# Kernel tuning notes

Hardware: AMD Instinct MI355X
Metric: run time of the kernel (lower is better)

Reference implementation:

```python
import jax, jax.numpy as jnp
import numpy as np

N_NODES = 100000
N_EDGES = 1600000
IN_CH, HID_CH, OUT_CH = 128, 128, 64


def setup_inputs() -> dict:
    key = jax.random.key(0)
    ks = jax.random.split(key, 9)
    x = jax.random.normal(ks[0], (N_NODES, IN_CH), dtype=jnp.float32)
    edge_index = jax.random.randint(ks[1], (2, N_EDGES), 0, N_NODES, dtype=jnp.int64)
    def glorot(k, shape):
        fan_in = shape[1]
        return jax.random.normal(k, shape, dtype=jnp.float32) / jnp.sqrt(jnp.float32(fan_in))
    return {
        "x": x,
        "edge_index": edge_index,
        "W1_l": glorot(ks[2], (HID_CH, IN_CH)),
        "W1_r": glorot(ks[3], (HID_CH, IN_CH)),
        "b1": jnp.zeros((HID_CH,), jnp.float32),
        "W2_l": glorot(ks[4], (HID_CH, HID_CH)),
        "W2_r": glorot(ks[5], (HID_CH, HID_CH)),
        "b2": jnp.zeros((HID_CH,), jnp.float32),
        "W3_l": glorot(ks[6], (OUT_CH, HID_CH)),
        "W3_r": glorot(ks[7], (OUT_CH, HID_CH)),
        "b3": jnp.zeros((OUT_CH,), jnp.float32),
    }


def _sage_conv(x, src, dst, W_l, W_r, b):
    # PyG SAGEConv (aggr='mean', root_weight=True): out = lin_l(mean_j x_j) + lin_r(x_i)
    n = x.shape[0]
    msg = x[src]                                            # [E, C] gather at source
    agg = jax.ops.segment_sum(msg, dst, num_segments=n)     # [N, C] scatter-sum at dest
    cnt = jax.ops.segment_sum(jnp.ones((src.shape[0],), x.dtype), dst, num_segments=n)
    mean = agg / jnp.maximum(cnt, 1.0)[:, None]             # zero-in-degree nodes -> 0
    return mean @ W_l.T + x @ W_r.T + b


def reference(x, edge_index, W1_l, W1_r, b1, W2_l, W2_r, b2, W3_l, W3_r, b3):
    src, dst = edge_index[0], edge_index[1]
    h = jax.nn.relu(_sage_conv(x, src, dst, W1_l, W1_r, b1))
    # F.dropout with training=False is identity (eval mode)
    h = jax.nn.relu(_sage_conv(h, src, dst, W2_l, W2_r, b2))
    return _sage_conv(h, src, dst, W3_l, W3_r, b3)
```

## Files before the change

kernel.cpp:

```cpp
#include <hip/hip_runtime.h>
#include <hip/hip_bf16.h>
#include <cstddef>
#include <cstdint>

#define NBLK(n, b) (((n) + (b) - 1) / (b))

typedef __attribute__((ext_vector_type(8))) short short8;
typedef __attribute__((ext_vector_type(4))) float f32x4;

__device__ inline unsigned short f2bf(float f) {
  union { float f; unsigned u; } v; v.f = f;
  unsigned u = v.u;
  u += 0x7FFFu + ((u >> 16) & 1u);
  return (unsigned short)(u >> 16);
}
__device__ inline float bflo(unsigned u) { union { unsigned u; float f; } v; v.u = u << 16; return v.f; }
__device__ inline float bfhi(unsigned u) { union { unsigned u; float f; } v; v.u = u & 0xFFFF0000u; return v.f; }

#define BSHIFT 9
#define BSIZE 512


__device__ inline void prep_w_dev(const float* __restrict__ Wl, const float* __restrict__ Wr,
                                  unsigned short* __restrict__ Wb, int b) {
  int i = b * 256 + threadIdx.x;
  int nrow = i >> 8, k = i & 255;
  float v = (k < 128) ? Wr[nrow * 128 + k] : Wl[nrow * 128 + (k - 128)];
  Wb[i] = f2bf(v);
}

__global__ void k_setup(const float* __restrict__ x, unsigned* __restrict__ xb, int N,
                        int* __restrict__ bucketCnt, int NB,
                        const float* __restrict__ W1l, const float* __restrict__ W1r, unsigned short* __restrict__ Wb1,
                        const float* __restrict__ W2l, const float* __restrict__ W2r, unsigned short* __restrict__ Wb2,
                        const float* __restrict__ W3l, const float* __restrict__ W3r, unsigned short* __restrict__ Wb3,
                        const unsigned* __restrict__ edges, int* __restrict__ flag) {
  int b = blockIdx.x;
  int gCast = (N * 64 + 255) >> 8;
  if (b < gCast) {
    int i = b * 256 + threadIdx.x;
    if (i < N * 64) {
      float2 v = *(const float2*)(x + (size_t)i * 2);
      xb[i] = (unsigned)f2bf(v.x) | ((unsigned)f2bf(v.y) << 16);
    }
    return;
  }
  b -= gCast;
  if (b < 128) { prep_w_dev(W1l, W1r, Wb1, b); return; }
  b -= 128;
  if (b < 128) { prep_w_dev(W2l, W2r, Wb2, b); return; }
  b -= 128;
  if (b < 64) { prep_w_dev(W3l, W3r, Wb3, b); return; }
  b -= 64;
  if (b == 0) {
    for (int i = threadIdx.x; i < NB; i += 256) bucketCnt[i] = 0;
    if (threadIdx.x == 0) {
      int is64 = 1;
#pragma unroll
      for (int i = 0; i < 16; ++i)
        if (edges[2 * i + 1] != 0u) is64 = 0;
      *flag = is64;
    }
  }
}


__global__ __launch_bounds__(256) void k_bhist(const void* __restrict__ edges, const int* __restrict__ flag,
                                               int* __restrict__ bucketCnt, int E, int NB) {
  __shared__ int h[1024];
  for (int i = threadIdx.x; i < NB; i += 256) h[i] = 0;
  __syncthreads();
  int base_e = blockIdx.x * 4096;
  bool is64 = (*flag) != 0;
#pragma unroll
  for (int k = 0; k < 16; ++k) {
    int e = base_e + k * 256 + threadIdx.x;
    if (e < E) {
      int d;
      if (is64) d = (int)((const long long*)edges)[(size_t)E + e];
      else      d = ((const int*)edges)[(size_t)E + e];
      atomicAdd(&h[d >> BSHIFT], 1);
    }
  }
  __syncthreads();
  for (int i = threadIdx.x; i < NB; i += 256) {
    int c = h[i];
    if (c) atomicAdd(&bucketCnt[i], c);
  }
}

__global__ void k_bscan(const int* __restrict__ bucketCnt, int* __restrict__ bucketBase,
                        int* __restrict__ bucketCursor, int NB, int E) {
  __shared__ int sd[256];
  int t = threadIdx.x;
  int base = t * 4;
  int v[4];
  int sum = 0;
#pragma unroll
  for (int i = 0; i < 4; ++i) {
    int idx = base + i;
    v[i] = (idx < NB) ? bucketCnt[idx] : 0;
    sum += v[i];
  }
  sd[t] = sum;
  __syncthreads();
  for (int off = 1; off < 256; off <<= 1) {
    int xv = (t >= off) ? sd[t - off] : 0;
    __syncthreads();
    sd[t] += xv;
    __syncthreads();
  }
  int run = sd[t] - sum;
#pragma unroll
  for (int i = 0; i < 4; ++i) {
    int idx = base + i;
    if (idx < NB) { bucketBase[idx] = run; bucketCursor[idx] = run; }
    run += v[i];
  }
  if (t == 0) bucketBase[NB] = E;
}

__global__ __launch_bounds__(256) void k_bscatter(const void* __restrict__ edges, const int* __restrict__ flag,
                                                  int* __restrict__ bucketCursor, unsigned* __restrict__ bucketed,
                                                  int E, int NB) {
  __shared__ int h[1024];
  __shared__ int base[1024];
  for (int i = threadIdx.x; i < NB; i += 256) h[i] = 0;
  __syncthreads();
  int base_e = blockIdx.x * 4096;
  bool is64 = (*flag) != 0;
  unsigned key[16];
  int bkt[16];
#pragma unroll
  for (int k = 0; k < 16; ++k) {
    int e = base_e + k * 256 + threadIdx.x;
    bkt[k] = -1;
    if (e < E) {
      int s, d;
      if (is64) {
        s = (int)((const long long*)edges)[e];
        d = (int)((const long long*)edges)[(size_t)E + e];
      } else {
        s = ((const int*)edges)[e];
        d = ((const int*)edges)[(size_t)E + e];
      }
      bkt[k] = d >> BSHIFT;
      key[k] = (unsigned)s | ((unsigned)(d & (BSIZE - 1)) << 17);
      atomicAdd(&h[bkt[k]], 1);
    }
  }
  __syncthreads();
  for (int i = threadIdx.x; i < NB; i += 256) {
    int c = h[i];
    base[i] = c ? atomicAdd(&bucketCursor[i], c) : 0;
    h[i] = 0;
  }
  __syncthreads();
#pragma unroll
  for (int k = 0; k < 16; ++k) {
    if (bkt[k] >= 0) {
      int r = atomicAdd(&h[bkt[k]], 1);
      bucketed[base[bkt[k]] + r] = key[k];
    }
  }
}

__global__ __launch_bounds__(256) void k_csr(const unsigned* __restrict__ bucketed,
                                             const int* __restrict__ bucketBase,
                                             int* __restrict__ rowptr, int* __restrict__ srcSorted,
                                             int N, int E, int NB) {
  __shared__ int h[512];
  __shared__ int excl[512];
  __shared__ int sd[256];
  int b = blockIdx.x;
  int t = threadIdx.x;
  int nodeBase = b << BSHIFT;
  int nNode = min(BSIZE, N - nodeBase);
  int s0 = bucketBase[b], s1 = bucketBase[b + 1];
  int cnt = s1 - s0;
  h[t * 2] = 0; h[t * 2 + 1] = 0;
  __syncthreads();
  for (int i = t; i < cnt; i += 256) {
    int ld = bucketed[s0 + i] >> 17;
    atomicAdd(&h[ld], 1);
  }
  __syncthreads();
  int a0 = h[t * 2], a1 = h[t * 2 + 1];
  int s = a0 + a1;
  sd[t] = s;
  __syncthreads();
  for (int off = 1; off < 256; off <<= 1) {
    int xv = (t >= off) ? sd[t - off] : 0;
    __syncthreads();
    sd[t] += xv;
    __syncthreads();
  }
  int run = sd[t] - s;
  excl[t * 2] = run;
  excl[t * 2 + 1] = run + a0;
  if (t * 2 < nNode) rowptr[nodeBase + t * 2] = s0 + run;
  if (t * 2 + 1 < nNode) rowptr[nodeBase + t * 2 + 1] = s0 + run + a0;
  if (b == NB - 1 && t == 0) rowptr[N] = E;
  h[t * 2] = 0; h[t * 2 + 1] = 0;
  __syncthreads();
  for (int i = t; i < cnt; i += 256) {
    unsigned u = bucketed[s0 + i];
    int ld = u >> 17;
    int r = atomicAdd(&h[ld], 1);
    srcSorted[s0 + excl[ld] + r] = (int)(u & 0x1FFFFu);
  }
}

__global__ void k_aggregate(const unsigned* __restrict__ in, const int* __restrict__ rowptr,
                            const int* __restrict__ srcs, unsigned* __restrict__ mean, int n) {
  int lane = threadIdx.x & 63;
  int w = threadIdx.x >> 6;
  int node = blockIdx.x * 4 + w;
  if (node >= n) return;
  int r0 = rowptr[node], r1 = rowptr[node + 1];
  int sub = lane & 15;
  int eg = lane >> 4;
  float acc[8];
#pragma unroll
  for (int k = 0; k < 8; ++k) acc[k] = 0.f;

  for (int base = r0; base < r1; base += 64) {
    int e = base + lane;
    int sv = (e < r1) ? srcs[e] : 0;
    int cnt = min(64, r1 - base);
    int j = 0;
    for (; j + 8 <= cnt; j += 8) {
      int s0 = __shfl(sv, j + eg);
      int s1 = __shfl(sv, j + 4 + eg);
      uint4 u0 = *(const uint4*)(in + (size_t)s0 * 64 + sub * 4);
      uint4 u1 = *(const uint4*)(in + (size_t)s1 * 64 + sub * 4);
      acc[0] += bflo(u0.x); acc[1] += bfhi(u0.x);
      acc[2] += bflo(u0.y); acc[3] += bfhi(u0.y);
      acc[4] += bflo(u0.z); acc[5] += bfhi(u0.z);
      acc[6] += bflo(u0.w); acc[7] += bfhi(u0.w);
      acc[0] += bflo(u1.x); acc[1] += bfhi(u1.x);
      acc[2] += bflo(u1.y); acc[3] += bfhi(u1.y);
      acc[4] += bflo(u1.z); acc[5] += bfhi(u1.z);
      acc[6] += bflo(u1.w); acc[7] += bfhi(u1.w);
    }
    for (; j < cnt; j += 4) {
      int jj = j + eg;
      int s = __shfl(sv, jj);
      if (jj < cnt) {
        uint4 u = *(const uint4*)(in + (size_t)s * 64 + sub * 4);
        acc[0] += bflo(u.x); acc[1] += bfhi(u.x);
        acc[2] += bflo(u.y); acc[3] += bfhi(u.y);
        acc[4] += bflo(u.z); acc[5] += bfhi(u.z);
        acc[6] += bflo(u.w); acc[7] += bfhi(u.w);
      }
    }
  }

#pragma unroll
  for (int k = 0; k < 8; ++k) {
    acc[k] += __shfl_down(acc[k], 32);
    acc[k] += __shfl_down(acc[k], 16);
  }
  if (eg == 0) {
    float sc = 1.0f / (float)max(r1 - r0, 1);
    uint4 o;
    o.x = (unsigned)f2bf(acc[0] * sc) | ((unsigned)f2bf(acc[1] * sc) << 16);
    o.y = (unsigned)f2bf(acc[2] * sc) | ((unsigned)f2bf(acc[3] * sc) << 16);
    o.z = (unsigned)f2bf(acc[4] * sc) | ((unsigned)f2bf(acc[5] * sc) << 16);
    o.w = (unsigned)f2bf(acc[6] * sc) | ((unsigned)f2bf(acc[7] * sc) << 16);
    *(uint4*)(mean + (size_t)node * 64 + sub * 4) = o;
  }
}

template <int H, bool RELU, bool BF16OUT>
__global__ __launch_bounds__(256) void k_gemm(
    const unsigned short* __restrict__ selfB, const unsigned short* __restrict__ meanB,
    const unsigned short* __restrict__ Wb, const float* __restrict__ bias,
    void* __restrict__ outp, int n) {
  constexpr int TN = H / 32;
  int lane = threadIdx.x & 63;
  int w = threadIdx.x >> 6;
  int wr = w & 1, wc = w >> 1;
  int nodeBase = blockIdx.x * 128 + wr * 64;
  int colBase = wc * (H / 2);
  int l15 = lane & 15, quad = lane >> 4;

  f32x4 acc[4][TN];
#pragma unroll
  for (int t = 0; t < 4; ++t)
#pragma unroll
    for (int j = 0; j < TN; ++j) acc[t][j] = (f32x4){0.f, 0.f, 0.f, 0.f};

#pragma unroll
  for (int c = 0; c < 8; ++c) {
    const unsigned short* A = (c < 4) ? selfB : meanB;
    int ko = (c & 3) * 32 + quad * 8;
    short8 af[4], bfr[TN];
#pragma unroll
    for (int t = 0; t < 4; ++t) {
      int row = nodeBase + t * 16 + l15;
      row = min(row, n - 1);
      af[t] = *(const short8*)(A + (size_t)row * 128 + ko);
    }
#pragma unroll
    for (int j = 0; j < TN; ++j) {
      int cn = colBase + j * 16 + l15;
      bfr[j] = *(const short8*)(Wb + (size_t)cn * 256 + c * 32 + quad * 8);
    }
#pragma unroll
    for (int t = 0; t < 4; ++t)
#pragma unroll
      for (int j = 0; j < TN; ++j)
        acc[t][j] = __builtin_amdgcn_mfma_f32_16x16x32_bf16(af[t], bfr[j], acc[t][j], 0, 0, 0);
  }

#pragma unroll
  for (int j = 0; j < TN; ++j) {
    int col = colBase + j * 16 + l15;
    float bv = bias[col];
#pragma unroll
    for (int t = 0; t < 4; ++t) {
#pragma unroll
      for (int r = 0; r < 4; ++r) {
        int row = nodeBase + t * 16 + quad * 4 + r;
        if (row < n) {
          float v = acc[t][j][r] + bv;
          if (RELU) v = fmaxf(v, 0.f);
          if (BF16OUT) ((unsigned short*)outp)[(size_t)row * H + col] = f2bf(v);
          else ((float*)outp)[(size_t)row * H + col] = v;
        }
      }
    }
  }
}


extern "C" void kernel_launch(void* const* d_in, const int* in_sizes, int n_in,
                              void* d_out, int out_size, void* d_ws, size_t ws_size,
                              hipStream_t stream) {
  (void)n_in; (void)out_size; (void)ws_size;
  const float* x = (const float*)d_in[0];
  const void* edges = d_in[1];
  const float* W1l = (const float*)d_in[2];
  const float* W1r = (const float*)d_in[3];
  const float* b1 = (const float*)d_in[4];
  const float* W2l = (const float*)d_in[5];
  const float* W2r = (const float*)d_in[6];
  const float* b2 = (const float*)d_in[7];
  const float* W3l = (const float*)d_in[8];
  const float* W3r = (const float*)d_in[9];
  const float* b3 = (const float*)d_in[10];
  float* out = (float*)d_out;

  const int N = in_sizes[0] / 128;
  const int E = in_sizes[1] / 2;
  const int NB = (N + BSIZE - 1) >> BSHIFT;

  char* ws = (char*)d_ws;
  size_t off = 0;
  auto alloc = [&](size_t bytes) -> char* {
    char* p = ws + off;
    off = (off + bytes + 255) & ~(size_t)255;
    return p;
  };
  int* flag = (int*)alloc(4);
  int* bucketCnt = (int*)alloc((size_t)NB * 4);
  int* bucketBase = (int*)alloc((size_t)(NB + 1) * 4);
  int* bucketCursor = (int*)alloc((size_t)NB * 4);
  unsigned* bucketed = (unsigned*)alloc((size_t)E * 4);
  int* rowptr = (int*)alloc((size_t)(N + 1) * 4);
  int* srcSorted = (int*)alloc((size_t)E * 4);
  unsigned short* xb = (unsigned short*)alloc((size_t)N * 128 * 2);
  unsigned short* mean = (unsigned short*)alloc((size_t)N * 128 * 2);
  unsigned short* h1 = (unsigned short*)alloc((size_t)N * 128 * 2);
  unsigned short* h2 = (unsigned short*)alloc((size_t)N * 128 * 2);
  unsigned short* Wb1 = (unsigned short*)alloc(128 * 256 * 2);
  unsigned short* Wb2 = (unsigned short*)alloc(128 * 256 * 2);
  unsigned short* Wb3 = (unsigned short*)alloc(64 * 256 * 2);

  int gSetup = NBLK(N * 64, 256) + 128 + 128 + 64 + 1;
  int gE = NBLK(E, 4096);

  k_setup<<<gSetup, 256, 0, stream>>>(x, (unsigned*)xb, N, bucketCnt, NB,
                                      W1l, W1r, Wb1, W2l, W2r, Wb2, W3l, W3r, Wb3,
                                      (const unsigned*)edges, flag);
  k_bhist<<<gE, 256, 0, stream>>>(edges, flag, bucketCnt, E, NB);
  k_bscan<<<1, 256, 0, stream>>>(bucketCnt, bucketBase, bucketCursor, NB, E);
  k_bscatter<<<gE, 256, 0, stream>>>(edges, flag, bucketCursor, bucketed, E, NB);
  k_csr<<<NB, 256, 0, stream>>>(bucketed, bucketBase, rowptr, srcSorted, N, E, NB);

  int gAgg = NBLK(N, 4);
  int gGemm = NBLK(N, 128);

  k_aggregate<<<gAgg, 256, 0, stream>>>((const unsigned*)xb, rowptr, srcSorted, (unsigned*)mean, N);
  k_gemm<128, true, true><<<gGemm, 256, 0, stream>>>(xb, mean, Wb1, b1, h1, N);
  k_aggregate<<<gAgg, 256, 0, stream>>>((const unsigned*)h1, rowptr, srcSorted, (unsigned*)mean, N);
  k_gemm<128, true, true><<<gGemm, 256, 0, stream>>>(h1, mean, Wb2, b2, h2, N);
  k_aggregate<<<gAgg, 256, 0, stream>>>((const unsigned*)h2, rowptr, srcSorted, (unsigned*)mean, N);
  k_gemm<64, false, false><<<gGemm, 256, 0, stream>>>(h2, mean, Wb3, b3, out, N);
}
```

Baseline: 472.5 us.

## Fuse CSR build stages into one cooperative kernel with grid syncs

Merges setup, bucket histogram, scan, scatter and CSR construction into a single cooperative kernel separated by grid-wide barriers. Each block keeps its per-bucket histogram and keys in registers and shared memory between phases, so the edges are read once instead of twice. This removes several kernel launches and one pass over the edge list, at the cost of a grid size fixed to the edge chunk count, which must stay co-resident. The aggregation loop also gains a 16-wide unrolled gather to keep more loads in flight.

```diff
diff --git a/kernel.cpp b/kernel.cpp
--- a/kernel.cpp
+++ b/kernel.cpp
@@ -1,7 +1,10 @@
 #include <hip/hip_runtime.h>
 #include <hip/hip_bf16.h>
+#include <hip/hip_cooperative_groups.h>
 #include <cstddef>
 #include <cstdint>
+
+namespace cg = cooperative_groups;
 
 #define NBLK(n, b) (((n) + (b) - 1) / (b))
 
@@ -19,121 +22,60 @@
 
 #define BSHIFT 9
 #define BSIZE 512
-
-
-__device__ inline void prep_w_dev(const float* __restrict__ Wl, const float* __restrict__ Wr,
-                                  unsigned short* __restrict__ Wb, int b) {
-  int i = b * 256 + threadIdx.x;
-  int nrow = i >> 8, k = i & 255;
-  float v = (k < 128) ? Wr[nrow * 128 + k] : Wl[nrow * 128 + (k - 128)];
-  Wb[i] = f2bf(v);
-}
-
-__global__ void k_setup(const float* __restrict__ x, unsigned* __restrict__ xb, int N,
-                        int* __restrict__ bucketCnt, int NB,
-                        const float* __restrict__ W1l, const float* __restrict__ W1r, unsigned short* __restrict__ Wb1,
-                        const float* __restrict__ W2l, const float* __restrict__ W2r, unsigned short* __restrict__ Wb2,
-                        const float* __restrict__ W3l, const float* __restrict__ W3r, unsigned short* __restrict__ Wb3,
-                        const unsigned* __restrict__ edges, int* __restrict__ flag) {
-  int b = blockIdx.x;
-  int gCast = (N * 64 + 255) >> 8;
-  if (b < gCast) {
-    int i = b * 256 + threadIdx.x;
-    if (i < N * 64) {
-      float2 v = *(const float2*)(x + (size_t)i * 2);
-      xb[i] = (unsigned)f2bf(v.x) | ((unsigned)f2bf(v.y) << 16);
-    }
-    return;
-  }
-  b -= gCast;
-  if (b < 128) { prep_w_dev(W1l, W1r, Wb1, b); return; }
-  b -= 128;
-  if (b < 128) { prep_w_dev(W2l, W2r, Wb2, b); return; }
-  b -= 128;
-  if (b < 64) { prep_w_dev(W3l, W3r, Wb3, b); return; }
-  b -= 64;
-  if (b == 0) {
-    for (int i = threadIdx.x; i < NB; i += 256) bucketCnt[i] = 0;
-    if (threadIdx.x == 0) {
-      int is64 = 1;
-#pragma unroll
-      for (int i = 0; i < 16; ++i)
-        if (edges[2 * i + 1] != 0u) is64 = 0;
-      *flag = is64;
-    }
-  }
-}
-
-
-__global__ __launch_bounds__(256) void k_bhist(const void* __restrict__ edges, const int* __restrict__ flag,
-                                               int* __restrict__ bucketCnt, int E, int NB) {
+#define ECHUNK 4096
+
+__global__ __launch_bounds__(256, 2) void k_build(
+    const float* __restrict__ x, unsigned* __restrict__ xb, int N,
+    const float* __restrict__ W1l, const float* __restrict__ W1r, unsigned short* __restrict__ Wb1,
+    const float* __restrict__ W2l, const float* __restrict__ W2r, unsigned short* __restrict__ Wb2,
+    const float* __restrict__ W3l, const float* __restrict__ W3r, unsigned short* __restrict__ Wb3,
+    const void* __restrict__ edges, int* __restrict__ flag,
+    int* __restrict__ bucketCnt, int* __restrict__ bucketBase, int* __restrict__ bucketCursor,
+    unsigned* __restrict__ bucketed, int* __restrict__ rowptr, int* __restrict__ srcSorted,
+    int E, int NB) {
+  cg::grid_group grid = cg::this_grid();
   __shared__ int h[1024];
-  for (int i = threadIdx.x; i < NB; i += 256) h[i] = 0;
-  __syncthreads();
-  int base_e = blockIdx.x * 4096;
-  bool is64 = (*flag) != 0;
-#pragma unroll
-  for (int k = 0; k < 16; ++k) {
-    int e = base_e + k * 256 + threadIdx.x;
-    if (e < E) {
-      int d;
-      if (is64) d = (int)((const long long*)edges)[(size_t)E + e];
-      else      d = ((const int*)edges)[(size_t)E + e];
-      atomicAdd(&h[d >> BSHIFT], 1);
-    }
-  }
-  __syncthreads();
-  for (int i = threadIdx.x; i < NB; i += 256) {
-    int c = h[i];
-    if (c) atomicAdd(&bucketCnt[i], c);
-  }
-}
-
-__global__ void k_bscan(const int* __restrict__ bucketCnt, int* __restrict__ bucketBase,
-                        int* __restrict__ bucketCursor, int NB, int E) {
+  __shared__ int base2[1024];
   __shared__ int sd[256];
   int t = threadIdx.x;
-  int base = t * 4;
-  int v[4];
-  int sum = 0;
-#pragma unroll
-  for (int i = 0; i < 4; ++i) {
-    int idx = base + i;
-    v[i] = (idx < NB) ? bucketCnt[idx] : 0;
-    sum += v[i];
-  }
-  sd[t] = sum;
+  int gid = blockIdx.x * 256 + t;
+  int gstride = gridDim.x * 256;
+
+  for (int i = gid; i < N * 64; i += gstride) {
+    float2 v = *(const float2*)(x + (size_t)i * 2);
+    xb[i] = (unsigned)f2bf(v.x) | ((unsigned)f2bf(v.y) << 16);
+  }
+  for (int i = gid; i < 320 * 256; i += gstride) {
+    const float *Wl, *Wr; unsigned short* Wb; int ii = i;
+    if (ii < 128 * 256) { Wl = W1l; Wr = W1r; Wb = Wb1; }
+    else if (ii < 256 * 256) { Wl = W2l; Wr = W2r; Wb = Wb2; ii -= 128 * 256; }
+    else { Wl = W3l; Wr = W3r; Wb = Wb3; ii -= 256 * 256; }
+    int nrow = ii >> 8, k = ii & 255;
+    float v = (k < 128) ? Wr[nrow * 128 + k] : Wl[nrow * 128 + (k - 128)];
+    Wb[ii] = f2bf(v);
+  }
+  if (blockIdx.x == 0) {
+    for (int i = t; i < NB; i += 256) bucketCnt[i] = 0;
+    if (t == 0) {
+      const unsigned* e32 = (const unsigned*)edges;
+      int is64 = 1;
+#pragma unroll
+      for (int i = 0; i < 16; ++i)
+        if (e32[2 * i + 1] != 0u) is64 = 0;
+      *flag = is64;
+    }
+  }
+  grid.sync();
+
+  bool is64 = (*flag) != 0;
+  for (int i = t; i < NB; i += 256) h[i] = 0;
   __syncthreads();
-  for (int off = 1; off < 256; off <<= 1) {
-    int xv = (t >= off) ? sd[t - off] : 0;
-    __syncthreads();
-    sd[t] += xv;
-    __syncthreads();
-  }
-  int run = sd[t] - sum;
-#pragma unroll
-  for (int i = 0; i < 4; ++i) {
-    int idx = base + i;
-    if (idx < NB) { bucketBase[idx] = run; bucketCursor[idx] = run; }
-    run += v[i];
-  }
-  if (t == 0) bucketBase[NB] = E;
-}
-
-__global__ __launch_bounds__(256) void k_bscatter(const void* __restrict__ edges, const int* __restrict__ flag,
-                                                  int* __restrict__ bucketCursor, unsigned* __restrict__ bucketed,
-                                                  int E, int NB) {
-  __shared__ int h[1024];
-  __shared__ int base[1024];
-  for (int i = threadIdx.x; i < NB; i += 256) h[i] = 0;
-  __syncthreads();
-  int base_e = blockIdx.x * 4096;
-  bool is64 = (*flag) != 0;
+  int base_e = blockIdx.x * ECHUNK;
   unsigned key[16];
   int bkt[16];
 #pragma unroll
   for (int k = 0; k < 16; ++k) {
-    int e = base_e + k * 256 + threadIdx.x;
+    int e = base_e + k * 256 + t;
     bkt[k] = -1;
     if (e < E) {
       int s, d;
@@ -150,9 +92,44 @@
     }
   }
   __syncthreads();
-  for (int i = threadIdx.x; i < NB; i += 256) {
+  for (int i = t; i < NB; i += 256) {
     int c = h[i];
-    base[i] = c ? atomicAdd(&bucketCursor[i], c) : 0;
+    if (c) atomicAdd(&bucketCnt[i], c);
+  }
+  grid.sync();
+
+  if (blockIdx.x == 0) {
+    int base = t * 4;
+    int v[4];
+    int sum = 0;
+#pragma unroll
+    for (int i = 0; i < 4; ++i) {
+      int idx = base + i;
+      v[i] = (idx < NB) ? bucketCnt[idx] : 0;
+      sum += v[i];
+    }
+    sd[t] = sum;
+    __syncthreads();
+    for (int off = 1; off < 256; off <<= 1) {
+      int xv = (t >= off) ? sd[t - off] : 0;
+      __syncthreads();
+      sd[t] += xv;
+      __syncthreads();
+    }
+    int run = sd[t] - sum;
+#pragma unroll
+    for (int i = 0; i < 4; ++i) {
+      int idx = base + i;
+      if (idx < NB) { bucketBase[idx] = run; bucketCursor[idx] = run; }
+      run += v[i];
+    }
+    if (t == 0) bucketBase[NB] = E;
+  }
+  grid.sync();
+
+  for (int i = t; i < NB; i += 256) {
+    int c = h[i];
+    base2[i] = c ? atomicAdd(&bucketCursor[i], c) : 0;
     h[i] = 0;
   }
   __syncthreads();
@@ -160,54 +137,48 @@
   for (int k = 0; k < 16; ++k) {
     if (bkt[k] >= 0) {
       int r = atomicAdd(&h[bkt[k]], 1);
-      bucketed[base[bkt[k]] + r] = key[k];
-    }
-  }
-}
-
-__global__ __launch_bounds__(256) void k_csr(const unsigned* __restrict__ bucketed,
-                                             const int* __restrict__ bucketBase,
-                                             int* __restrict__ rowptr, int* __restrict__ srcSorted,
-                                             int N, int E, int NB) {
-  __shared__ int h[512];
-  __shared__ int excl[512];
-  __shared__ int sd[256];
+      bucketed[base2[bkt[k]] + r] = key[k];
+    }
+  }
+  grid.sync();
+
   int b = blockIdx.x;
-  int t = threadIdx.x;
-  int nodeBase = b << BSHIFT;
-  int nNode = min(BSIZE, N - nodeBase);
-  int s0 = bucketBase[b], s1 = bucketBase[b + 1];
-  int cnt = s1 - s0;
-  h[t * 2] = 0; h[t * 2 + 1] = 0;
-  __syncthreads();
-  for (int i = t; i < cnt; i += 256) {
-    int ld = bucketed[s0 + i] >> 17;
-    atomicAdd(&h[ld], 1);
-  }
-  __syncthreads();
-  int a0 = h[t * 2], a1 = h[t * 2 + 1];
-  int s = a0 + a1;
-  sd[t] = s;
-  __syncthreads();
-  for (int off = 1; off < 256; off <<= 1) {
-    int xv = (t >= off) ? sd[t - off] : 0;
+  if (b < NB) {
+    int nodeBase = b << BSHIFT;
+    int nNode = min(BSIZE, N - nodeBase);
+    int s0 = bucketBase[b], s1 = bucketBase[b + 1];
+    int cnt = s1 - s0;
+    h[t * 2] = 0; h[t * 2 + 1] = 0;
     __syncthreads();
-    sd[t] += xv;
+    for (int i = t; i < cnt; i += 256) {
+      int ld = bucketed[s0 + i] >> 17;
+      atomicAdd(&h[ld], 1);
+    }
     __syncthreads();
-  }
-  int run = sd[t] - s;
-  excl[t * 2] = run;
-  excl[t * 2 + 1] = run + a0;
-  if (t * 2 < nNode) rowptr[nodeBase + t * 2] = s0 + run;
-  if (t * 2 + 1 < nNode) rowptr[nodeBase + t * 2 + 1] = s0 + run + a0;
-  if (b == NB - 1 && t == 0) rowptr[N] = E;
-  h[t * 2] = 0; h[t * 2 + 1] = 0;
-  __syncthreads();
-  for (int i = t; i < cnt; i += 256) {
-    unsigned u = bucketed[s0 + i];
-    int ld = u >> 17;
-    int r = atomicAdd(&h[ld], 1);
-    srcSorted[s0 + excl[ld] + r] = (int)(u & 0x1FFFFu);
+    int a0 = h[t * 2], a1 = h[t * 2 + 1];
+    int s = a0 + a1;
+    sd[t] = s;
+    __syncthreads();
+    for (int off = 1; off < 256; off <<= 1) {
+      int xv = (t >= off) ? sd[t - off] : 0;
+      __syncthreads();
+      sd[t] += xv;
+      __syncthreads();
+    }
+    int run = sd[t] - s;
+    base2[t * 2] = run;
+    base2[t * 2 + 1] = run + a0;
+    if (t * 2 < nNode) rowptr[nodeBase + t * 2] = s0 + run;
+    if (t * 2 + 1 < nNode) rowptr[nodeBase + t * 2 + 1] = s0 + run + a0;
+    if (b == NB - 1 && t == 0) rowptr[N] = E;
+    h[t * 2] = 0; h[t * 2 + 1] = 0;
+    __syncthreads();
+    for (int i = t; i < cnt; i += 256) {
+      unsigned u = bucketed[s0 + i];
+      int ld = u >> 17;
+      int r = atomicAdd(&h[ld], 1);
+      srcSorted[s0 + base2[ld] + r] = (int)(u & 0x1FFFFu);
+    }
   }
 }
 
@@ -229,6 +200,32 @@
     int sv = (e < r1) ? srcs[e] : 0;
     int cnt = min(64, r1 - base);
     int j = 0;
+    for (; j + 16 <= cnt; j += 16) {
+      int s0 = __shfl(sv, j + eg);
+      int s1 = __shfl(sv, j + 4 + eg);
+      int s2 = __shfl(sv, j + 8 + eg);
+      int s3 = __shfl(sv, j + 12 + eg);
+      uint4 u0 = *(const uint4*)(in + (size_t)s0 * 64 + sub * 4);
+      uint4 u1 = *(const uint4*)(in + (size_t)s1 * 64 + sub * 4);
+      uint4 u2 = *(const uint4*)(in + (size_t)s2 * 64 + sub * 4);
+      uint4 u3 = *(const uint4*)(in + (size_t)s3 * 64 + sub * 4);
+      acc[0] += bflo(u0.x); acc[1] += bfhi(u0.x);
+      acc[2] += bflo(u0.y); acc[3] += bfhi(u0.y);
+      acc[4] += bflo(u0.z); acc[5] += bfhi(u0.z);
+      acc[6] += bflo(u0.w); acc[7] += bfhi(u0.w);
+      acc[0] += bflo(u1.x); acc[1] += bfhi(u1.x);
+      acc[2] += bflo(u1.y); acc[3] += bfhi(u1.y);
+      acc[4] += bflo(u1.z); acc[5] += bfhi(u1.z);
+      acc[6] += bflo(u1.w); acc[7] += bfhi(u1.w);
+      acc[0] += bflo(u2.x); acc[1] += bfhi(u2.x);
+      acc[2] += bflo(u2.y); acc[3] += bfhi(u2.y);
+      acc[4] += bflo(u2.z); acc[5] += bfhi(u2.z);
+      acc[6] += bflo(u2.w); acc[7] += bfhi(u2.w);
+      acc[0] += bflo(u3.x); acc[1] += bfhi(u3.x);
+      acc[2] += bflo(u3.y); acc[3] += bfhi(u3.y);
+      acc[4] += bflo(u3.z); acc[5] += bfhi(u3.z);
+      acc[6] += bflo(u3.w); acc[7] += bfhi(u3.w);
+    }
     for (; j + 8 <= cnt; j += 8) {
       int s0 = __shfl(sv, j + eg);
       int s1 = __shfl(sv, j + 4 + eg);
@@ -378,16 +375,22 @@
   unsigned short* Wb2 = (unsigned short*)alloc(128 * 256 * 2);
   unsigned short* Wb3 = (unsigned short*)alloc(64 * 256 * 2);
 
-  int gSetup = NBLK(N * 64, 256) + 128 + 128 + 64 + 1;
-  int gE = NBLK(E, 4096);
-
-  k_setup<<<gSetup, 256, 0, stream>>>(x, (unsigned*)xb, N, bucketCnt, NB,
-                                      W1l, W1r, Wb1, W2l, W2r, Wb2, W3l, W3r, Wb3,
-                                      (const unsigned*)edges, flag);
-  k_bhist<<<gE, 256, 0, stream>>>(edges, flag, bucketCnt, E, NB);
-  k_bscan<<<1, 256, 0, stream>>>(bucketCnt, bucketBase, bucketCursor, NB, E);
-  k_bscatter<<<gE, 256, 0, stream>>>(edges, flag, bucketCursor, bucketed, E, NB);
-  k_csr<<<NB, 256, 0, stream>>>(bucketed, bucketBase, rowptr, srcSorted, N, E, NB);
+  int gE = NBLK(E, ECHUNK);
+
+  {
+    const float* ax = x; unsigned* axb = (unsigned*)xb; int aN = N;
+    const float* a1l = W1l; const float* a1r = W1r; unsigned short* aw1 = Wb1;
+    const float* a2l = W2l; const float* a2r = W2r; unsigned short* aw2 = Wb2;
+    const float* a3l = W3l; const float* a3r = W3r; unsigned short* aw3 = Wb3;
+    const void* aed = edges; int* afl = flag;
+    int* abc = bucketCnt; int* abb = bucketBase; int* acu = bucketCursor;
+    unsigned* abk = bucketed; int* arp = rowptr; int* ass = srcSorted;
+    int aE = E; int aNB = NB;
+    void* args[] = { &ax, &axb, &aN,
+                     &a1l, &a1r, &aw1, &a2l, &a2r, &aw2, &a3l, &a3r, &aw3,
+                     &aed, &afl, &abc, &abb, &acu, &abk, &arp, &ass, &aE, &aNB };
+    hipLaunchCooperativeKernel((void*)k_build, dim3(gE), dim3(256), args, 0, stream);
+  }
 
   int gAgg = NBLK(N, 4);
   int gGemm = NBLK(N, 128);
```

Measured after the change: 690.0 us. 46.0% more time.
